# Kernel tuning notes

Measured on AMD Instinct MI355X. Metric: run time of the kernel, lower is better.

Reference implementation:

```python
import jax, jax.numpy as jnp
import numpy as np

N = 384          # nodes per graph
HID = 128        # hid_dim
H = 8            # shared_num_heads
C = HID // H     # shared_head_dim = 16
L = 4            # num_layers
VOCAB = 20
NORB = 4
NCAT = NORB * NORB + NORB   # 20 edge categories
OUT = 10
B = 4
E = N * N        # fully-connected closure incl. self loops
EPS = 1e-5


def layer_norm(x, g, b):
    m = jnp.mean(x, axis=-1, keepdims=True)
    v = jnp.mean((x - m) ** 2, axis=-1, keepdims=True)
    return (x - m) / jnp.sqrt(v + EPS) * g + b


def setup_inputs() -> dict:
    key = jax.random.key(0)
    ks = iter(jax.random.split(key, 32))

    def nrm(shape, s=0.05):
        return jax.random.normal(next(ks), shape, jnp.float32) * s

    # edge structure: fully connected, edge (i,j) in row-major order
    pos = np.arange(N) % NORB                    # node -> orbit
    src = np.repeat(np.arange(N), N)
    tgt = np.tile(np.arange(N), N)
    cat = np.where(src == tgt, NORB * NORB + pos[src], pos[src] * NORB + pos[tgt])

    x = jax.random.randint(next(ks), (B, N, 1), 0, VOCAB, jnp.int32)

    return dict(
        x=x,
        edge_src=jnp.asarray(src, jnp.int32),
        edge_tgt=jnp.asarray(tgt, jnp.int32),
        edge_cat=jnp.asarray(cat, jnp.int32),
        token_emb=nrm((VOCAB, HID), 1.0),
        edge_emb=nrm((NCAT, HID), 1.0),
        ln_in1_g=jnp.ones((HID,), jnp.float32), ln_in1_b=jnp.zeros((HID,), jnp.float32),
        W_in=nrm((HID, HID)), b_in=jnp.zeros((HID,), jnp.float32),
        ln_in2_g=jnp.ones((HID,), jnp.float32), ln_in2_b=jnp.zeros((HID,), jnp.float32),
        Wl=nrm((L, HID, H * C)), bl=jnp.zeros((L, H * C), jnp.float32),
        Wr=nrm((L, HID, H * C)), br=jnp.zeros((L, H * C), jnp.float32),
        We=nrm((L, HID, H * C)),                           # lin_edge has no bias in PyG GATv2Conv
        att=nrm((L, H, C)),
        bias_gat=jnp.zeros((L, H * C), jnp.float32),
        W_proj=nrm((L, HID, HID)), b_proj=jnp.zeros((L, HID), jnp.float32),
        ln_g=jnp.ones((L, HID), jnp.float32), ln_b=jnp.zeros((L, HID), jnp.float32),
        W_out=nrm((HID, OUT)), b_out=jnp.zeros((OUT,), jnp.float32),
    )


def reference(x, edge_src, edge_tgt, edge_cat,
              token_emb, edge_emb,
              ln_in1_g, ln_in1_b, W_in, b_in, ln_in2_g, ln_in2_b,
              Wl, bl, Wr, br, We, att, bias_gat,
              W_proj, b_proj, ln_g, ln_b, W_out, b_out):
    edge_feat = edge_emb[edge_cat]                       # [E, HID] gather by category
    h = token_emb[x[..., 0]]                             # [B, N, HID]
    # input MLP: LN -> ReLU -> Linear -> LN
    h = layer_norm(h, ln_in1_g, ln_in1_b)
    h = jax.nn.relu(h)
    h = h @ W_in + b_in
    h = layer_norm(h, ln_in2_g, ln_in2_b)

    for l in range(L):
        edge_e = (edge_feat @ We[l]).reshape(E, H, C)    # shared across batch

        def conv(hb):  # hb: [N, HID]  GATv2Conv, concat heads
            xl = (hb @ Wl[l] + bl[l]).reshape(N, H, C)   # source transform
            xr = (hb @ Wr[l] + br[l]).reshape(N, H, C)   # target transform
            e = jax.nn.leaky_relu(xl[edge_src] + xr[edge_tgt] + edge_e, 0.2)  # [E,H,C]
            logits = jnp.einsum('ehc,hc->eh', e, att[l])                      # [E,H]
            # segment softmax over edges sharing a target node
            m = jax.ops.segment_max(logits, edge_tgt, num_segments=N)
            ex = jnp.exp(logits - m[edge_tgt])
            den = jax.ops.segment_sum(ex, edge_tgt, num_segments=N)
            alpha = ex / den[edge_tgt]                                        # [E,H]
            out = jax.ops.segment_sum(xl[edge_src] * alpha[:, :, None], edge_tgt,
                                      num_segments=N)                         # [N,H,C]
            return out.reshape(N, H * C) + bias_gat[l]

        h_prev = h
        h = jax.vmap(conv)(h)                            # [B, N, HID]
        h = h @ W_proj[l] + b_proj[l]
        h = layer_norm(h, ln_g[l], ln_b[l])
        h = jax.nn.relu(h) + h_prev                      # residual

    h = h.sum(axis=1)                                    # sum over nodes -> [B, HID]
    return h @ W_out + b_out                             # [B, OUT]
```

## Files before the change

kernel.cpp:

```cpp
#include <hip/hip_runtime.h>


#define NN 384
#define NB 4
#define TJ 2

__device__ __forceinline__ void reduce64(float& a, float& b) {
#pragma unroll
  for (int m = 1; m <= 32; m <<= 1) {
    a += __shfl_xor(a, m, 64);
    b += __shfl_xor(b, m, 64);
  }
}

__global__ __launch_bounds__(256) void k_init(
    const int* __restrict__ x,
    const float* __restrict__ token_emb, const float* __restrict__ edge_emb,
    const float* __restrict__ ln1g, const float* __restrict__ ln1b,
    const float* __restrict__ W_in, const float* __restrict__ b_in,
    const float* __restrict__ ln2g, const float* __restrict__ ln2b,
    const float* __restrict__ Wl, const float* __restrict__ bl,
    const float* __restrict__ Wr, const float* __restrict__ br,
    const float* __restrict__ We, const float* __restrict__ att_w,
    float* __restrict__ ce, float* __restrict__ h,
    float* __restrict__ xl, float* __restrict__ xr, float* __restrict__ datt0)
{
  const int blk = blockIdx.x, t = threadIdx.x;
  if (blk < 40) {
    const int idx = blk * 256 + t;
    const int hc = idx & 127, rest = idx >> 7;
    const int cat = rest % 20, l = rest / 20;
    const float* er = edge_emb + cat * 128;
    const float* w  = We + (l * 128) * 128 + hc;
    float acc = 0.f;
#pragma unroll 8
    for (int k = 0; k < 128; ++k) acc = fmaf(er[k], w[k * 128], acc);
    ce[idx] = acc;
    return;
  }
  __shared__ float trow[4][128];
  __shared__ float hbuf[4][128];
  const int r0 = (blk - 40) * 4;
  const int r = t >> 6, c2 = (t & 63) * 2;
  const int row = r0 + r;
  const int tok = x[row];
  float2 v = *(const float2*)(token_emb + tok * 128 + c2);
  float s1 = v.x + v.y;
  float s2 = v.x * v.x + v.y * v.y;
  reduce64(s1, s2);
  float mean = s1 * 0.0078125f;
  float inv  = rsqrtf(s2 * 0.0078125f - mean * mean + 1e-5f);
  {
    float2 g  = *(const float2*)(ln1g + c2);
    float2 bb = *(const float2*)(ln1b + c2);
    trow[r][c2 + 0] = fmaxf((v.x - mean) * inv * g.x + bb.x, 0.f);
    trow[r][c2 + 1] = fmaxf((v.y - mean) * inv * g.y + bb.y, 0.f);
  }
  __syncthreads();
  const int o = t & 127, rh = (t >> 7) * 2;
  {
    float a0, a1;
    { float bo = b_in[o]; a0 = a1 = bo; }
    for (int k = 0; k < 128; ++k) {
      float w = W_in[k * 128 + o];
      a0 = fmaf(trow[rh + 0][k], w, a0);
      a1 = fmaf(trow[rh + 1][k], w, a1);
    }
    hbuf[rh + 0][o] = a0; hbuf[rh + 1][o] = a1;
  }
  __syncthreads();
  v = *(const float2*)(&hbuf[r][c2]);
  s1 = v.x + v.y;
  s2 = v.x * v.x + v.y * v.y;
  reduce64(s1, s2);
  mean = s1 * 0.0078125f;
  inv  = rsqrtf(s2 * 0.0078125f - mean * mean + 1e-5f);
  {
    float2 g  = *(const float2*)(ln2g + c2);
    float2 bb = *(const float2*)(ln2b + c2);
    float2 hv;
    hv.x = (v.x - mean) * inv * g.x + bb.x;
    hv.y = (v.y - mean) * inv * g.y + bb.y;
    trow[r][c2] = hv.x; trow[r][c2 + 1] = hv.y;
    *(float2*)(h + row * 128 + c2) = hv;
  }
  __syncthreads();
  const int m = t >> 7;
  const float* W = m ? Wr : Wl;
  const float bias = (m ? br : bl)[o];
  float a0 = bias, a1 = bias, a2 = bias, a3 = bias;
  for (int k = 0; k < 128; ++k) {
    float wv = W[k * 128 + o];
    a0 = fmaf(trow[0][k], wv, a0);
    a1 = fmaf(trow[1][k], wv, a1);
    a2 = fmaf(trow[2][k], wv, a2);
    a3 = fmaf(trow[3][k], wv, a3);
  }
  float* dst = m ? xr : xl;
  dst[(r0 + 0) * 128 + o] = a0;
  dst[(r0 + 1) * 128 + o] = a1;
  dst[(r0 + 2) * 128 + o] = a2;
  dst[(r0 + 3) * 128 + o] = a3;
  if (m == 0) {
    float av = att_w[o];
    float s0 = av * a0, sA = av * a1, sB = av * a2, sC = av * a3;
#pragma unroll
    for (int mm = 1; mm <= 8; mm <<= 1) {
      s0 += __shfl_xor(s0, mm, 64);
      sA += __shfl_xor(sA, mm, 64);
      sB += __shfl_xor(sB, mm, 64);
      sC += __shfl_xor(sC, mm, 64);
    }
    if ((t & 15) == 0) {
      const int hh2 = o >> 4;
      const int b2 = r0 / NN, ii = r0 - b2 * NN;
      const int base = (b2 * 8 + hh2) * NN + ii;
      datt0[base + 0] = s0; datt0[base + 1] = sA;
      datt0[base + 2] = sB; datt0[base + 3] = sC;
    }
  }
}

__global__ __launch_bounds__(256) void k_layer(
    const float* __restrict__ xl_in, const float* __restrict__ xr_in,
    const float* __restrict__ datt_in,
    float* __restrict__ xl_out, float* __restrict__ xr_out,
    float* __restrict__ datt_out,
    float* __restrict__ h, const float* __restrict__ ce,
    const float* __restrict__ att_w, const float* __restrict__ bias_gat,
    const float* __restrict__ W_proj, const float* __restrict__ b_proj,
    const float* __restrict__ ln_g, const float* __restrict__ ln_b,
    const float* __restrict__ Wl, const float* __restrict__ bl,
    const float* __restrict__ Wr, const float* __restrict__ br,
    int l, int next_l)
{
  __shared__ float xrce[TJ][5][136];
  __shared__ float djr02[TJ][5][8];
  __shared__ float mbuf[8][32][17];
  __shared__ float arow[TJ][132];
  __shared__ float pbuf[2 * TJ][132];
  __shared__ float nrow[TJ][132];

  const int t = threadIdx.x;
  const int jt = blockIdx.x, b = blockIdx.y;
  const int j0 = jt * TJ;

  for (int idx = t; idx < TJ * 5 * 128; idx += 256) {
    const int hc = idx & 127, rest = idx >> 7;
    const int sel = rest % 5, jj = rest / 5;
    const int j = j0 + jj, pj = j & 3;
    const int cat = (sel == 4) ? (16 + pj) : (sel * 4 + pj);
    xrce[jj][sel][hc] = xr_in[(b * NN + j) * 128 + hc]
                      + ce[(l * 20 + cat) * 128 + hc];
  }
  __syncthreads();
  if (t < TJ * 5 * 8) {
    const int jj = t / 40, r2 = t % 40, sel = r2 >> 3, h2 = r2 & 7;
    float d = 0.f;
#pragma unroll
    for (int c = 0; c < 16; ++c)
      d += xrce[jj][sel][h2 * 16 + c] * att_w[l * 128 + h2 * 16 + c];
    djr02[jj][sel][h2] = 0.2f * d;
  }
  __syncthreads();

  const int hh = t >> 5, isub = t & 31;
  float attv[16];
  {
    const float* ap = att_w + l * 128 + hh * 16;
#pragma unroll
    for (int c = 0; c < 16; ++c) attv[c] = ap[c];
  }
  const int pfix = isub & 3;
  float cvj[TJ][16], djf[TJ];
#pragma unroll
  for (int jj = 0; jj < TJ; ++jj) {
    const float4* cp = (const float4*)(&xrce[jj][pfix][hh * 16]);
#pragma unroll
    for (int q = 0; q < 4; ++q) {
      float4 cv = cp[q];
      cvj[jj][q * 4 + 0] = cv.x; cvj[jj][q * 4 + 1] = cv.y;
      cvj[jj][q * 4 + 2] = cv.z; cvj[jj][q * 4 + 3] = cv.w;
    }
    djf[jj] = djr02[jj][pfix][hh];
  }
  float sden[TJ];
  float acc[TJ][16];
#pragma unroll
  for (int jj = 0; jj < TJ; ++jj) {
    sden[jj] = 0.f;
#pragma unroll
    for (int c = 0; c < 16; ++c) acc[jj][c] = 0.f;
  }
  const float* xlb = xl_in + (b * NN) * 128 + hh * 16;
  const float* dp  = datt_in + (b * 8 + hh) * NN;

#pragma unroll 2
  for (int it = 0; it < NN / 32; ++it) {
    const int i = isub + 32 * it;
    float xv[16];
    {
      const float4* xp = (const float4*)(xlb + i * 128);
#pragma unroll
      for (int q = 0; q < 4; ++q) {
        float4 a = xp[q];
        xv[q * 4 + 0] = a.x; xv[q * 4 + 1] = a.y;
        xv[q * 4 + 2] = a.z; xv[q * 4 + 3] = a.w;
      }
    }
    const float di02 = 0.2f * dp[i];
#pragma unroll
    for (int jj = 0; jj < TJ; ++jj) {
      float p = 0.f;
#pragma unroll
      for (int c = 0; c < 16; ++c)
        p = fmaf(fmaxf(xv[c] + cvj[jj][c], 0.f), attv[c], p);
      float dj = djf[jj];
      if (i == j0 + jj) {
        const float* b4 = &xrce[jj][4][hh * 16];
        float ps = 0.f;
#pragma unroll
        for (int c = 0; c < 16; ++c)
          ps = fmaf(fmaxf(xv[c] + b4[c], 0.f), attv[c], ps);
        p = ps;
        dj = djr02[jj][4][hh];
      }
      const float e = __expf(fmaf(0.8f, p, di02 + dj));
      sden[jj] += e;
#pragma unroll
      for (int c = 0; c < 16; ++c) acc[jj][c] = fmaf(e, xv[c], acc[jj][c]);
    }
  }

  {
    const int lc = isub & 15, up = isub >> 4;
#pragma unroll
    for (int jj = 0; jj < TJ; ++jj) {
      mbuf[hh][isub][0] = sden[jj];
#pragma unroll
      for (int c = 0; c < 16; ++c) mbuf[hh][isub][1 + c] = acc[jj][c];
      float nsum = 0.f, dsum = 0.f;
#pragma unroll 4
      for (int u2 = 0; u2 < 16; ++u2) {
        const int u = up * 16 + u2;
        dsum += mbuf[hh][u][0];
        nsum += mbuf[hh][u][1 + lc];
      }
      nsum += __shfl_xor(nsum, 16, 64); dsum += __shfl_xor(dsum, 16, 64);
      if (isub < 16)
        arow[jj][hh * 16 + isub] =
            nsum / dsum + bias_gat[l * 128 + hh * 16 + isub];
    }
  }
  __syncthreads();

  {
    const int o = t & 127, g4 = t >> 7;
    const float* Wp = W_proj + l * 16384;
    float p0 = 0.f, p1 = 0.f;
    const int k0 = g4 * 64;
    for (int kk = 0; kk < 64; ++kk) {
      const int k = k0 + kk;
      const float w = Wp[k * 128 + o];
      p0 = fmaf(arow[0][k], w, p0);
      p1 = fmaf(arow[1][k], w, p1);
    }
    pbuf[g4 * 2 + 0][o] = p0;
    pbuf[g4 * 2 + 1][o] = p1;
  }
  __syncthreads();
  {
    const int rr = t >> 7, o = t & 127;
    nrow[rr][o] = pbuf[rr][o] + pbuf[2 + rr][o] + b_proj[l * 128 + o];
  }
  __syncthreads();

  {
    const int w = t >> 6;
    if (w < TJ) {
      const int c2 = (t & 63) * 2;
      float v0 = nrow[w][c2], v1 = nrow[w][c2 + 1];
      float s1 = v0 + v1, s2 = v0 * v0 + v1 * v1;
#pragma unroll
      for (int m = 1; m <= 32; m <<= 1) {
        s1 += __shfl_xor(s1, m, 64);
        s2 += __shfl_xor(s2, m, 64);
      }
      const float mean = s1 * 0.0078125f;
      const float inv  = rsqrtf(s2 * 0.0078125f - mean * mean + 1e-5f);
      const int row = (b * NN + j0 + w) * 128;
      const float g0 = ln_g[l * 128 + c2], g1 = ln_g[l * 128 + c2 + 1];
      const float b0 = ln_b[l * 128 + c2], b1 = ln_b[l * 128 + c2 + 1];
      const float hp0 = h[row + c2], hp1 = h[row + c2 + 1];
      const float hn0 = fmaxf((v0 - mean) * inv * g0 + b0, 0.f) + hp0;
      const float hn1 = fmaxf((v1 - mean) * inv * g1 + b1, 0.f) + hp1;
      h[row + c2] = hn0; h[row + c2 + 1] = hn1;
      nrow[w][c2] = hn0; nrow[w][c2 + 1] = hn1;
    }
  }
  __syncthreads();

  if (next_l >= 0) {
    const int o = t & 127, m = t >> 7;
    const float* W = (m ? Wr : Wl) + next_l * 16384;
    const float bias = (m ? br : bl)[next_l * 128 + o];
    float a0 = bias, a1 = bias;
    for (int k = 0; k < 128; ++k) {
      const float wv = W[k * 128 + o];
      a0 = fmaf(nrow[0][k], wv, a0);
      a1 = fmaf(nrow[1][k], wv, a1);
    }
    float* dst = m ? xr_out : xl_out;
    const int rb = (b * NN + j0) * 128 + o;
    dst[rb] = a0; dst[rb + 128] = a1;
    if (m == 0) {
      const float av = att_w[next_l * 128 + o];
      float s0 = av * a0, s1 = av * a1;
#pragma unroll
      for (int mm = 1; mm <= 8; mm <<= 1) {
        s0 += __shfl_xor(s0, mm, 64);
        s1 += __shfl_xor(s1, mm, 64);
      }
      if ((t & 15) == 0) {
        const int base = (b * 8 + (o >> 4)) * NN + j0;
        datt_out[base + 0] = s0;
        datt_out[base + 1] = s1;
      }
    }
  }
}

__global__ __launch_bounds__(256) void k_final(
    const float* __restrict__ h, const float* __restrict__ W_out,
    const float* __restrict__ b_out, float* __restrict__ out)
{
  __shared__ float sbuf[2][128];
  const int bq = blockIdx.x, t = threadIdx.x;
  const int o = t & 127, half = t >> 7;
  float acc = 0.f;
  const float* hp = h + (bq * NN + half * 192) * 128 + o;
  for (int n = 0; n < 192; ++n) acc += hp[n * 128];
  sbuf[half][o] = acc;
  __syncthreads();
  if (t < 10) {
    float a = b_out[t];
#pragma unroll 8
    for (int k = 0; k < 128; ++k)
      a = fmaf(sbuf[0][k] + sbuf[1][k], W_out[k * 10 + t], a);
    out[bq * 10 + t] = a;
  }
}

extern "C" void kernel_launch(void* const* d_in, const int* in_sizes, int n_in,
                              void* d_out, int out_size, void* d_ws, size_t ws_size,
                              hipStream_t stream) {
  const int*   x         = (const int*)d_in[0];
  const float* token_emb = (const float*)d_in[4];
  const float* edge_emb  = (const float*)d_in[5];
  const float* ln1g      = (const float*)d_in[6];
  const float* ln1b      = (const float*)d_in[7];
  const float* W_in      = (const float*)d_in[8];
  const float* b_in      = (const float*)d_in[9];
  const float* ln2g      = (const float*)d_in[10];
  const float* ln2b      = (const float*)d_in[11];
  const float* Wl        = (const float*)d_in[12];
  const float* bl        = (const float*)d_in[13];
  const float* Wr        = (const float*)d_in[14];
  const float* br        = (const float*)d_in[15];
  const float* We        = (const float*)d_in[16];
  const float* att_w     = (const float*)d_in[17];
  const float* bias_gat  = (const float*)d_in[18];
  const float* W_proj    = (const float*)d_in[19];
  const float* b_proj    = (const float*)d_in[20];
  const float* ln_g      = (const float*)d_in[21];
  const float* ln_b      = (const float*)d_in[22];
  const float* W_out     = (const float*)d_in[23];
  const float* b_out     = (const float*)d_in[24];

  float* ws  = (float*)d_ws;
  float* ce  = ws;
  float* h   = ce  + 10240;
  float* xlA = h   + 196608;
  float* xrA = xlA + 196608;
  float* xlB = xrA + 196608;
  float* xrB = xlB + 196608;
  float* dA  = xrB + 196608;
  float* dB  = dA  + 12288;

  k_init<<<dim3(40 + 384), 256, 0, stream>>>(
      x, token_emb, edge_emb, ln1g, ln1b, W_in, b_in, ln2g, ln2b,
      Wl, bl, Wr, br, We, att_w, ce, h, xlA, xrA, dA);
  for (int l = 0; l < 4; ++l) {
    const bool even = (l & 1) == 0;
    float* xin  = even ? xlA : xlB;  float* rin  = even ? xrA : xrB;
    float* din  = even ? dA  : dB;
    float* xout = even ? xlB : xlA;  float* rout = even ? xrB : xrA;
    float* dout = even ? dB  : dA;
    k_layer<<<dim3(NN / TJ, NB), 256, 0, stream>>>(
        xin, rin, din, xout, rout, dout, h, ce, att_w, bias_gat,
        W_proj, b_proj, ln_g, ln_b, Wl, bl, Wr, br, l, (l < 3) ? l + 1 : -1);
  }
  k_final<<<dim3(NB), 256, 0, stream>>>(h, W_out, b_out, (float*)d_out);
}
```

Before: 237.5 us.

## Process four target nodes per block and read edge terms from LDS inside loop

Raises the number of target nodes per block from two to four, so each loaded source row xl and each weight row in the projection and next-layer GEMVs is reused across more targets. The per-thread preloaded cvj/djf register arrays are dropped; the edge-category term is now read from shared memory on each iteration, with a select that folds in the self-loop case. This halves the grid size and the weight reloads per layer. In exchange it adds LDS traffic in the inner loop, more accumulator registers (4x16), and fewer blocks to fill the GPU.

```diff
diff --git a/kernel.cpp b/kernel.cpp
--- a/kernel.cpp
+++ b/kernel.cpp
@@ -3,7 +3,7 @@
 
 #define NN 384
 #define NB 4
-#define TJ 2
+#define TJ 4
 
 __device__ __forceinline__ void reduce64(float& a, float& b) {
 #pragma unroll
@@ -171,19 +171,6 @@
 #pragma unroll
     for (int c = 0; c < 16; ++c) attv[c] = ap[c];
   }
-  const int pfix = isub & 3;
-  float cvj[TJ][16], djf[TJ];
-#pragma unroll
-  for (int jj = 0; jj < TJ; ++jj) {
-    const float4* cp = (const float4*)(&xrce[jj][pfix][hh * 16]);
-#pragma unroll
-    for (int q = 0; q < 4; ++q) {
-      float4 cv = cp[q];
-      cvj[jj][q * 4 + 0] = cv.x; cvj[jj][q * 4 + 1] = cv.y;
-      cvj[jj][q * 4 + 2] = cv.z; cvj[jj][q * 4 + 3] = cv.w;
-    }
-    djf[jj] = djr02[jj][pfix][hh];
-  }
   float sden[TJ];
   float acc[TJ][16];
 #pragma unroll
@@ -209,23 +196,21 @@
       }
     }
     const float di02 = 0.2f * dp[i];
+    const int pi = i & 3;
 #pragma unroll
     for (int jj = 0; jj < TJ; ++jj) {
+      const int sel = (i == j0 + jj) ? 4 : pi;
+      const float4* bp = (const float4*)(&xrce[jj][sel][hh * 16]);
       float p = 0.f;
 #pragma unroll
-      for (int c = 0; c < 16; ++c)
-        p = fmaf(fmaxf(xv[c] + cvj[jj][c], 0.f), attv[c], p);
-      float dj = djf[jj];
-      if (i == j0 + jj) {
-        const float* b4 = &xrce[jj][4][hh * 16];
-        float ps = 0.f;
-#pragma unroll
-        for (int c = 0; c < 16; ++c)
-          ps = fmaf(fmaxf(xv[c] + b4[c], 0.f), attv[c], ps);
-        p = ps;
-        dj = djr02[jj][4][hh];
-      }
-      const float e = __expf(fmaf(0.8f, p, di02 + dj));
+      for (int q = 0; q < 4; ++q) {
+        float4 cv = bp[q];
+        p = fmaf(fmaxf(xv[q * 4 + 0] + cv.x, 0.f), attv[q * 4 + 0], p);
+        p = fmaf(fmaxf(xv[q * 4 + 1] + cv.y, 0.f), attv[q * 4 + 1], p);
+        p = fmaf(fmaxf(xv[q * 4 + 2] + cv.z, 0.f), attv[q * 4 + 2], p);
+        p = fmaf(fmaxf(xv[q * 4 + 3] + cv.w, 0.f), attv[q * 4 + 3], p);
+      }
+      const float e = __expf(fmaf(0.8f, p, di02 + djr02[jj][sel][hh]));
       sden[jj] += e;
 #pragma unroll
       for (int c = 0; c < 16; ++c) acc[jj][c] = fmaf(e, xv[c], acc[jj][c]);
@@ -257,46 +242,48 @@
   {
     const int o = t & 127, g4 = t >> 7;
     const float* Wp = W_proj + l * 16384;
-    float p0 = 0.f, p1 = 0.f;
+    float p0 = 0.f, p1 = 0.f, p2 = 0.f, p3 = 0.f;
     const int k0 = g4 * 64;
     for (int kk = 0; kk < 64; ++kk) {
       const int k = k0 + kk;
       const float w = Wp[k * 128 + o];
       p0 = fmaf(arow[0][k], w, p0);
       p1 = fmaf(arow[1][k], w, p1);
-    }
-    pbuf[g4 * 2 + 0][o] = p0;
-    pbuf[g4 * 2 + 1][o] = p1;
-  }
-  __syncthreads();
-  {
-    const int rr = t >> 7, o = t & 127;
-    nrow[rr][o] = pbuf[rr][o] + pbuf[2 + rr][o] + b_proj[l * 128 + o];
+      p2 = fmaf(arow[2][k], w, p2);
+      p3 = fmaf(arow[3][k], w, p3);
+    }
+    pbuf[g4 * TJ + 0][o] = p0;
+    pbuf[g4 * TJ + 1][o] = p1;
+    pbuf[g4 * TJ + 2][o] = p2;
+    pbuf[g4 * TJ + 3][o] = p3;
+  }
+  __syncthreads();
+  for (int idx = t; idx < TJ * 128; idx += 256) {
+    const int rr = idx >> 7, o = idx & 127;
+    nrow[rr][o] = pbuf[rr][o] + pbuf[TJ + rr][o] + b_proj[l * 128 + o];
   }
   __syncthreads();
 
   {
     const int w = t >> 6;
-    if (w < TJ) {
-      const int c2 = (t & 63) * 2;
-      float v0 = nrow[w][c2], v1 = nrow[w][c2 + 1];
-      float s1 = v0 + v1, s2 = v0 * v0 + v1 * v1;
-#pragma unroll
-      for (int m = 1; m <= 32; m <<= 1) {
-        s1 += __shfl_xor(s1, m, 64);
-        s2 += __shfl_xor(s2, m, 64);
-      }
-      const float mean = s1 * 0.0078125f;
-      const float inv  = rsqrtf(s2 * 0.0078125f - mean * mean + 1e-5f);
-      const int row = (b * NN + j0 + w) * 128;
-      const float g0 = ln_g[l * 128 + c2], g1 = ln_g[l * 128 + c2 + 1];
-      const float b0 = ln_b[l * 128 + c2], b1 = ln_b[l * 128 + c2 + 1];
-      const float hp0 = h[row + c2], hp1 = h[row + c2 + 1];
-      const float hn0 = fmaxf((v0 - mean) * inv * g0 + b0, 0.f) + hp0;
-      const float hn1 = fmaxf((v1 - mean) * inv * g1 + b1, 0.f) + hp1;
-      h[row + c2] = hn0; h[row + c2 + 1] = hn1;
-      nrow[w][c2] = hn0; nrow[w][c2 + 1] = hn1;
-    }
+    const int c2 = (t & 63) * 2;
+    float v0 = nrow[w][c2], v1 = nrow[w][c2 + 1];
+    float s1 = v0 + v1, s2 = v0 * v0 + v1 * v1;
+#pragma unroll
+    for (int m = 1; m <= 32; m <<= 1) {
+      s1 += __shfl_xor(s1, m, 64);
+      s2 += __shfl_xor(s2, m, 64);
+    }
+    const float mean = s1 * 0.0078125f;
+    const float inv  = rsqrtf(s2 * 0.0078125f - mean * mean + 1e-5f);
+    const int row = (b * NN + j0 + w) * 128;
+    const float g0 = ln_g[l * 128 + c2], g1 = ln_g[l * 128 + c2 + 1];
+    const float b0 = ln_b[l * 128 + c2], b1 = ln_b[l * 128 + c2 + 1];
+    const float hp0 = h[row + c2], hp1 = h[row + c2 + 1];
+    const float hn0 = fmaxf((v0 - mean) * inv * g0 + b0, 0.f) + hp0;
+    const float hn1 = fmaxf((v1 - mean) * inv * g1 + b1, 0.f) + hp1;
+    h[row + c2] = hn0; h[row + c2 + 1] = hn1;
+    nrow[w][c2] = hn0; nrow[w][c2 + 1] = hn1;
   }
   __syncthreads();
 
@@ -304,27 +291,34 @@
     const int o = t & 127, m = t >> 7;
     const float* W = (m ? Wr : Wl) + next_l * 16384;
     const float bias = (m ? br : bl)[next_l * 128 + o];
-    float a0 = bias, a1 = bias;
+    float a0 = bias, a1 = bias, a2 = bias, a3 = bias;
     for (int k = 0; k < 128; ++k) {
       const float wv = W[k * 128 + o];
       a0 = fmaf(nrow[0][k], wv, a0);
       a1 = fmaf(nrow[1][k], wv, a1);
+      a2 = fmaf(nrow[2][k], wv, a2);
+      a3 = fmaf(nrow[3][k], wv, a3);
     }
     float* dst = m ? xr_out : xl_out;
     const int rb = (b * NN + j0) * 128 + o;
-    dst[rb] = a0; dst[rb + 128] = a1;
+    dst[rb +   0] = a0; dst[rb + 128] = a1;
+    dst[rb + 256] = a2; dst[rb + 384] = a3;
     if (m == 0) {
       const float av = att_w[next_l * 128 + o];
-      float s0 = av * a0, s1 = av * a1;
+      float s0 = av * a0, s1 = av * a1, s2 = av * a2, s3 = av * a3;
 #pragma unroll
       for (int mm = 1; mm <= 8; mm <<= 1) {
         s0 += __shfl_xor(s0, mm, 64);
         s1 += __shfl_xor(s1, mm, 64);
+        s2 += __shfl_xor(s2, mm, 64);
+        s3 += __shfl_xor(s3, mm, 64);
       }
       if ((t & 15) == 0) {
         const int base = (b * 8 + (o >> 4)) * NN + j0;
         datt_out[base + 0] = s0;
         datt_out[base + 1] = s1;
+        datt_out[base + 2] = s2;
+        datt_out[base + 3] = s3;
       }
     }
   }
```

Result: no change. 236.9 us (-0.2%).
